# Optimization experiments

Measured on AMD Instinct MI355X. Metric: run time of the kernel, lower is better.

The kernel has to match this reference:

```python
import jax, jax.numpy as jnp
import numpy as np

B, N, IN, OUT, H = 8, 1024, 256, 256, 4
D = OUT // H  # head_dim = 64


def setup_inputs() -> dict:
    key = jax.random.key(0)
    k1, k2, k3, k4 = jax.random.split(key, 4)
    h = jax.random.normal(k1, (B, N, IN), dtype=jnp.float32)
    # torch Linear weight: [out, in], Wh = h @ W.T
    W = jax.random.normal(k2, (H * D, IN), dtype=jnp.float32) * (1.0 / np.sqrt(IN))
    # attention vector a: [n_heads, 2*head_dim] (xavier-uniform-ish scale)
    a = jax.random.normal(k3, (H, 2 * D), dtype=jnp.float32) * 0.1
    adj_mask = jax.random.bernoulli(k4, 0.1, (B, N, N))
    # ensure every row has at least one neighbor (self-loop) to avoid all -inf rows
    adj_mask = adj_mask | jnp.eye(N, dtype=bool)[None]
    return {"h": h, "W": W, "a": a, "adj_mask": adj_mask}


def reference(h, W, a, adj_mask):
    # Wh: [B, H, N, D]
    Wh = (h @ W.T).reshape(B, N, H, D).transpose(0, 2, 1, 3)
    # Split 'a' into src/dst halves: e_ij = leaky_relu(a_src.Wh_i + a_dst.Wh_j)
    # (mathematically identical to the original concat+einsum, without the N^2*2D tensor)
    src = jnp.einsum('bhnd,hd->bhn', Wh, a[:, :D])
    dst = jnp.einsum('bhnd,hd->bhn', Wh, a[:, D:])
    e = jax.nn.leaky_relu(src[:, :, :, None] + dst[:, :, None, :], negative_slope=0.2)
    e = jnp.where(adj_mask[:, None, :, :], e, -jnp.inf)
    att = jax.nn.softmax(e, axis=-1)
    att = jnp.where(jnp.isnan(att), 0.0, att)
    # dropout in eval mode -> identity
    h_prime = jnp.einsum('bhij,bhjd->bhid', att, Wh)
    # concat=True: [B, N, H*D]
    return h_prime.transpose(0, 2, 1, 3).reshape(B, N, H * D)
```

## Files before the change

kernel.cpp:

```cpp
#include <hip/hip_runtime.h>
#include <hip/hip_bf16.h>

#define B 8
#define N 1024
#define IN 256
#define H 4
#define D 64
#define O 256
#define BN (B*N)

typedef __attribute__((ext_vector_type(4))) float f32x4;
typedef __attribute__((ext_vector_type(8))) short short8;
typedef __attribute__((ext_vector_type(4))) short short4v;

__device__ __forceinline__ short f2bf(float f){
  __hip_bfloat16 b = __float2bfloat16(f);
  return __builtin_bit_cast(short, b);
}
__device__ __forceinline__ float bf2f(short s){
  unsigned u = ((unsigned)(unsigned short)s) << 16;
  return __builtin_bit_cast(float, u);
}

__global__ __launch_bounds__(256) void k_wh(const float* __restrict__ hmat,
                                            const float* __restrict__ Wmat,
                                            short* __restrict__ VT){
  const int t = threadIdx.x;
  const int wave = t >> 6, lane = t & 63, quad = lane >> 4, l16 = lane & 15;
  const int msub = blockIdx.x * 32 + (wave >> 1) * 16;
  const int obase = (wave & 1) * 128;
  f32x4 acc[8];
  #pragma unroll
  for(int x=0;x<8;x++) acc[x] = (f32x4){0.f,0.f,0.f,0.f};
  const float* ap = hmat + (size_t)(msub + l16) * IN + quad * 8;
  for(int k0 = 0; k0 < IN; k0 += 32){
    float4 a0 = *(const float4*)(ap + k0);
    float4 a1 = *(const float4*)(ap + k0 + 4);
    short8 A;
    A[0]=f2bf(a0.x); A[1]=f2bf(a0.y); A[2]=f2bf(a0.z); A[3]=f2bf(a0.w);
    A[4]=f2bf(a1.x); A[5]=f2bf(a1.y); A[6]=f2bf(a1.z); A[7]=f2bf(a1.w);
    #pragma unroll
    for(int dt=0; dt<8; dt++){
      const float* bp = Wmat + (size_t)(obase + dt*16 + l16) * IN + k0 + quad*8;
      float4 b0 = *(const float4*)bp;
      float4 b1 = *(const float4*)(bp + 4);
      short8 Bf;
      Bf[0]=f2bf(b0.x); Bf[1]=f2bf(b0.y); Bf[2]=f2bf(b0.z); Bf[3]=f2bf(b0.w);
      Bf[4]=f2bf(b1.x); Bf[5]=f2bf(b1.y); Bf[6]=f2bf(b1.z); Bf[7]=f2bf(b1.w);
      acc[dt] = __builtin_amdgcn_mfma_f32_16x16x32_bf16(A, Bf, acc[dt], 0, 0, 0);
    }
  }
  const int bb = msub >> 10;
  const int nb = (msub & (N-1)) + quad * 4;
  #pragma unroll
  for(int dt=0; dt<8; dt++){
    int o = obase + dt*16 + l16;
    int hh = o >> 6, d = o & 63;
    short4v pk;
    pk[0]=f2bf(acc[dt][0]); pk[1]=f2bf(acc[dt][1]);
    pk[2]=f2bf(acc[dt][2]); pk[3]=f2bf(acc[dt][3]);
    *(short4v*)(VT + (((size_t)(bb*H + hh)*D + d) << 10) + nb) = pk;
  }
}

__global__ __launch_bounds__(256) void k_srcdst(const short* __restrict__ VT,
                                                const float* __restrict__ avec,
                                                float* __restrict__ src,
                                                float* __restrict__ dst){
  int t = blockIdx.x * 256 + threadIdx.x;
  int bh = t >> 10, n = t & (N-1);
  int hh = bh & (H-1);
  const float* av = avec + hh * (2*D);
  const short* vp = VT + ((size_t)bh << 16) + n;
  float s = 0.f, dd = 0.f;
  #pragma unroll 8
  for(int d=0; d<D; d++){
    float v = bf2f(vp[(size_t)d << 10]);
    s  += v * av[d];
    dd += v * av[D + d];
  }
  src[t] = s; dst[t] = dd;
}

__global__ __launch_bounds__(256) void k_attn(const short* __restrict__ VT,
                                              const float* __restrict__ src,
                                              const float* __restrict__ dst,
                                              const int* __restrict__ adj,
                                              float* __restrict__ out){
  __shared__ float dsh[N];
  __shared__ short vt[D * 40];
  __shared__ float lsh[4][16];
  const int t = threadIdx.x;
  const int wave = t >> 6, lane = t & 63, quad = lane >> 4, l16 = lane & 15;
  const int b = blockIdx.z, hh = blockIdx.y;
  const int bh = b * H + hh;
  const int i0 = blockIdx.x * 64;
  for(int j = t; j < N; j += 256) dsh[j] = dst[(size_t)bh * N + j];
  const int i = i0 + wave * 16 + l16;
  const float si = src[(size_t)bh * N + i];
  const int* adjrow = adj + ((size_t)b * N + i) * N;
  const int sd = t >> 2;
  const int sc = (t & 3) * 8;
  const short* vsrc = VT + (((size_t)bh * D + sd) << 10) + sc;
  f32x4 acc[4];
  #pragma unroll
  for(int x=0;x<4;x++) acc[x] = (f32x4){0.f,0.f,0.f,0.f};
  float lsum = 0.f;
  for(int j0 = 0; j0 < N; j0 += 32){
    __syncthreads();
    *(short8*)&vt[sd * 40 + sc] = *(const short8*)(vsrc + j0);
    __syncthreads();
    const int4* amp = (const int4*)(adjrow + j0 + quad * 8);
    int4 m0 = amp[0], m1 = amp[1];
    int msk[8] = {m0.x, m0.y, m0.z, m0.w, m1.x, m1.y, m1.z, m1.w};
    short8 P;
    #pragma unroll
    for(int jj=0; jj<8; jj++){
      float e = si + dsh[j0 + quad*8 + jj];
      e = e > 0.f ? e : 0.2f * e;
      float p = msk[jj] ? __expf(e) : 0.f;
      P[jj] = f2bf(p);
      lsum += bf2f(P[jj]);
    }
    #pragma unroll
    for(int dt=0; dt<4; dt++){
      short8 Bf = *(const short8*)&vt[(dt*16 + l16) * 40 + quad*8];
      acc[dt] = __builtin_amdgcn_mfma_f32_16x16x32_bf16(P, Bf, acc[dt], 0, 0, 0);
    }
  }
  lsum += __shfl_xor(lsum, 16, 64);
  lsum += __shfl_xor(lsum, 32, 64);
  if(quad == 0) lsh[wave][l16] = lsum;
  __syncthreads();
  #pragma unroll
  for(int dt=0; dt<4; dt++){
    #pragma unroll
    for(int r=0; r<4; r++){
      int irow = quad * 4 + r;
      float inv = 1.0f / lsh[wave][irow];
      int ig = i0 + wave * 16 + irow;
      out[((size_t)b * N + ig) * O + hh * D + dt * 16 + l16] = acc[dt][r] * inv;
    }
  }
}

extern "C" void kernel_launch(void* const* d_in, const int* in_sizes, int n_in,
                              void* d_out, int out_size, void* d_ws, size_t ws_size,
                              hipStream_t stream) {
  const float* hmat = (const float*)d_in[0];
  const float* Wmat = (const float*)d_in[1];
  const float* avec = (const float*)d_in[2];
  const int* adj    = (const int*)d_in[3];
  float* out = (float*)d_out;
  short* VT  = (short*)d_ws;
  float* src = (float*)((char*)d_ws + (size_t)4*1024*1024);
  float* dst = src + (size_t)B*H*N;
  k_wh<<<BN/32, 256, 0, stream>>>(hmat, Wmat, VT);
  k_srcdst<<<(B*H*N)/256, 256, 0, stream>>>(VT, avec, src, dst);
  k_attn<<<dim3(N/64, H, B), 256, 0, stream>>>(VT, src, dst, adj, out);
}
```

Baseline: 154.0 us.

## Pack adjacency to bitmask, pre-convert to bf16, fuse src/dst, split-K attention

Adds a prep kernel that packs the int32 adjacency mask into bits and converts h and W to bf16 once. The projection GEMM now computes the src/dst attention dot products in its epilogue, which removes a separate kernel. The attention kernel is split into two j-halves, reads V directly from global memory instead of staging it in shared memory, and writes partial sums that a new combine kernel reduces. The intent is to stop re-reading the 4-byte mask once per head and to increase the number of blocks, at the cost of an extra pass and the partial-sum traffic.

Result: faster. 138.1 us (-10.3%).

```diff
diff --git a/kernel.cpp b/kernel.cpp
--- a/kernel.cpp
+++ b/kernel.cpp
@@ -22,126 +22,179 @@
   return __builtin_bit_cast(float, u);
 }
 
-__global__ __launch_bounds__(256) void k_wh(const float* __restrict__ hmat,
-                                            const float* __restrict__ Wmat,
-                                            short* __restrict__ VT){
+#define PACK_BLOCKS 1024
+#define CVT_BLOCKS  1056
+#define H_ELEMS (BN*IN)
+__global__ __launch_bounds__(256) void k_prep(const int* __restrict__ adj,
+                                              unsigned* __restrict__ bits,
+                                              const float* __restrict__ hmat,
+                                              const float* __restrict__ Wmat,
+                                              short* __restrict__ hbf,
+                                              short* __restrict__ wbf){
+  if(blockIdx.x < PACK_BLOCKS){
+    int t = blockIdx.x * 256 + threadIdx.x;
+    const int4* p = (const int4*)(adj + ((size_t)t << 5));
+    unsigned word = 0;
+    #pragma unroll
+    for(int k = 0; k < 8; k++){
+      int4 m = p[k];
+      word |= (m.x != 0 ? 1u : 0u) << (k*4 + 0);
+      word |= (m.y != 0 ? 1u : 0u) << (k*4 + 1);
+      word |= (m.z != 0 ? 1u : 0u) << (k*4 + 2);
+      word |= (m.w != 0 ? 1u : 0u) << (k*4 + 3);
+    }
+    bits[t] = word;
+  } else {
+    int idx = (blockIdx.x - PACK_BLOCKS) * 256 + threadIdx.x;
+    int e = idx * 8;
+    const float* srcp; short* dstp;
+    if(e < H_ELEMS){ srcp = hmat + e; dstp = hbf + e; }
+    else           { srcp = Wmat + (e - H_ELEMS); dstp = wbf + (e - H_ELEMS); }
+    float4 a0 = *(const float4*)srcp;
+    float4 a1 = *(const float4*)(srcp + 4);
+    short8 pk;
+    pk[0]=f2bf(a0.x); pk[1]=f2bf(a0.y); pk[2]=f2bf(a0.z); pk[3]=f2bf(a0.w);
+    pk[4]=f2bf(a1.x); pk[5]=f2bf(a1.y); pk[6]=f2bf(a1.z); pk[7]=f2bf(a1.w);
+    *(short8*)dstp = pk;
+  }
+}
+
+__global__ __launch_bounds__(256) void k_wh(const short* __restrict__ hbf,
+                                            const short* __restrict__ wbf,
+                                            const float* __restrict__ avec,
+                                            short* __restrict__ VT,
+                                            float* __restrict__ src,
+                                            float* __restrict__ dst){
   const int t = threadIdx.x;
-  const int wave = t >> 6, lane = t & 63, quad = lane >> 4, l16 = lane & 15;
-  const int msub = blockIdx.x * 32 + (wave >> 1) * 16;
-  const int obase = (wave & 1) * 128;
-  f32x4 acc[8];
-  #pragma unroll
-  for(int x=0;x<8;x++) acc[x] = (f32x4){0.f,0.f,0.f,0.f};
-  const float* ap = hmat + (size_t)(msub + l16) * IN + quad * 8;
-  for(int k0 = 0; k0 < IN; k0 += 32){
-    float4 a0 = *(const float4*)(ap + k0);
-    float4 a1 = *(const float4*)(ap + k0 + 4);
-    short8 A;
-    A[0]=f2bf(a0.x); A[1]=f2bf(a0.y); A[2]=f2bf(a0.z); A[3]=f2bf(a0.w);
-    A[4]=f2bf(a1.x); A[5]=f2bf(a1.y); A[6]=f2bf(a1.z); A[7]=f2bf(a1.w);
-    #pragma unroll
-    for(int dt=0; dt<8; dt++){
-      const float* bp = Wmat + (size_t)(obase + dt*16 + l16) * IN + k0 + quad*8;
-      float4 b0 = *(const float4*)bp;
-      float4 b1 = *(const float4*)(bp + 4);
-      short8 Bf;
-      Bf[0]=f2bf(b0.x); Bf[1]=f2bf(b0.y); Bf[2]=f2bf(b0.z); Bf[3]=f2bf(b0.w);
-      Bf[4]=f2bf(b1.x); Bf[5]=f2bf(b1.y); Bf[6]=f2bf(b1.z); Bf[7]=f2bf(b1.w);
+  const int hh = t >> 6, lane = t & 63, quad = lane >> 4, l16 = lane & 15;
+  const int mbase = blockIdx.x * 16;
+  f32x4 acc[4];
+  #pragma unroll
+  for(int x=0;x<4;x++) acc[x] = (f32x4){0.f,0.f,0.f,0.f};
+  const short* ap = hbf + (size_t)(mbase + l16) * IN + quad * 8;
+  const short* bp0 = wbf + (size_t)(hh * 64 + l16) * IN + quad * 8;
+  #pragma unroll
+  for(int kk = 0; kk < 8; kk++){
+    const int k0 = kk * 32;
+    short8 A = *(const short8*)(ap + k0);
+    #pragma unroll
+    for(int dt=0; dt<4; dt++){
+      short8 Bf = *(const short8*)(bp0 + (size_t)dt*16*IN + k0);
       acc[dt] = __builtin_amdgcn_mfma_f32_16x16x32_bf16(A, Bf, acc[dt], 0, 0, 0);
     }
   }
-  const int bb = msub >> 10;
-  const int nb = (msub & (N-1)) + quad * 4;
-  #pragma unroll
-  for(int dt=0; dt<8; dt++){
-    int o = obase + dt*16 + l16;
-    int hh = o >> 6, d = o & 63;
+  const int bb = mbase >> 10;
+  const int nb = (mbase & (N-1)) + quad * 4;
+  const int bh = bb * H + hh;
+  #pragma unroll
+  for(int dt=0; dt<4; dt++){
+    int d = dt*16 + l16;
     short4v pk;
     pk[0]=f2bf(acc[dt][0]); pk[1]=f2bf(acc[dt][1]);
     pk[2]=f2bf(acc[dt][2]); pk[3]=f2bf(acc[dt][3]);
-    *(short4v*)(VT + (((size_t)(bb*H + hh)*D + d) << 10) + nb) = pk;
-  }
-}
-
-__global__ __launch_bounds__(256) void k_srcdst(const short* __restrict__ VT,
-                                                const float* __restrict__ avec,
-                                                float* __restrict__ src,
-                                                float* __restrict__ dst){
-  int t = blockIdx.x * 256 + threadIdx.x;
-  int bh = t >> 10, n = t & (N-1);
-  int hh = bh & (H-1);
-  const float* av = avec + hh * (2*D);
-  const short* vp = VT + ((size_t)bh << 16) + n;
-  float s = 0.f, dd = 0.f;
-  #pragma unroll 8
-  for(int d=0; d<D; d++){
-    float v = bf2f(vp[(size_t)d << 10]);
-    s  += v * av[d];
-    dd += v * av[D + d];
-  }
-  src[t] = s; dst[t] = dd;
+    *(short4v*)(VT + (((size_t)bh * D + d) << 10) + nb) = pk;
+  }
+  float as[4], ad[4];
+  #pragma unroll
+  for(int dt=0; dt<4; dt++){
+    as[dt] = avec[hh*(2*D) + dt*16 + l16];
+    ad[dt] = avec[hh*(2*D) + D + dt*16 + l16];
+  }
+  #pragma unroll
+  for(int r=0; r<4; r++){
+    float s = 0.f, dd = 0.f;
+    #pragma unroll
+    for(int dt=0; dt<4; dt++){ s += acc[dt][r]*as[dt]; dd += acc[dt][r]*ad[dt]; }
+    #pragma unroll
+    for(int off=1; off<16; off<<=1){
+      s  += __shfl_xor(s, off, 64);
+      dd += __shfl_xor(dd, off, 64);
+    }
+    if(l16 == 0){
+      int n = nb + r;
+      src[(size_t)bh * N + n] = s;
+      dst[(size_t)bh * N + n] = dd;
+    }
+  }
 }
 
 __global__ __launch_bounds__(256) void k_attn(const short* __restrict__ VT,
                                               const float* __restrict__ src,
                                               const float* __restrict__ dst,
-                                              const int* __restrict__ adj,
-                                              float* __restrict__ out){
-  __shared__ float dsh[N];
-  __shared__ short vt[D * 40];
-  __shared__ float lsh[4][16];
+                                              const unsigned* __restrict__ bits,
+                                              float* __restrict__ pacc,
+                                              float* __restrict__ plsum){
+  __shared__ float dsh[512];
   const int t = threadIdx.x;
   const int wave = t >> 6, lane = t & 63, quad = lane >> 4, l16 = lane & 15;
   const int b = blockIdx.z, hh = blockIdx.y;
   const int bh = b * H + hh;
-  const int i0 = blockIdx.x * 64;
-  for(int j = t; j < N; j += 256) dsh[j] = dst[(size_t)bh * N + j];
+  const int ib = blockIdx.x >> 1, jc = blockIdx.x & 1;
+  const int i0 = ib * 64, jbase = jc * 512;
+  #pragma unroll
+  for(int j = t; j < 512; j += 256) dsh[j] = dst[(size_t)bh * N + jbase + j];
   const int i = i0 + wave * 16 + l16;
   const float si = src[(size_t)bh * N + i];
-  const int* adjrow = adj + ((size_t)b * N + i) * N;
-  const int sd = t >> 2;
-  const int sc = (t & 3) * 8;
-  const short* vsrc = VT + (((size_t)bh * D + sd) << 10) + sc;
+  const int4* mp = (const int4*)(bits + ((size_t)b * N + i) * 32 + jc * 16);
+  int4 mv0 = mp[0], mv1 = mp[1], mv2 = mp[2], mv3 = mp[3];
+  unsigned mw[16] = {(unsigned)mv0.x,(unsigned)mv0.y,(unsigned)mv0.z,(unsigned)mv0.w,
+                     (unsigned)mv1.x,(unsigned)mv1.y,(unsigned)mv1.z,(unsigned)mv1.w,
+                     (unsigned)mv2.x,(unsigned)mv2.y,(unsigned)mv2.z,(unsigned)mv2.w,
+                     (unsigned)mv3.x,(unsigned)mv3.y,(unsigned)mv3.z,(unsigned)mv3.w};
+  const short* vrow = VT + (((size_t)bh * D) << 10) + jbase + quad * 8;
   f32x4 acc[4];
   #pragma unroll
   for(int x=0;x<4;x++) acc[x] = (f32x4){0.f,0.f,0.f,0.f};
   float lsum = 0.f;
-  for(int j0 = 0; j0 < N; j0 += 32){
-    __syncthreads();
-    *(short8*)&vt[sd * 40 + sc] = *(const short8*)(vsrc + j0);
-    __syncthreads();
-    const int4* amp = (const int4*)(adjrow + j0 + quad * 8);
-    int4 m0 = amp[0], m1 = amp[1];
-    int msk[8] = {m0.x, m0.y, m0.z, m0.w, m1.x, m1.y, m1.z, m1.w};
+  __syncthreads();
+  #pragma unroll
+  for(int jt = 0; jt < 16; jt++){
+    const int j0 = jt * 32;
+    const unsigned word = mw[jt];
+    float4 d0 = *(const float4*)&dsh[j0 + quad*8];
+    float4 d1 = *(const float4*)&dsh[j0 + quad*8 + 4];
+    float dv[8] = {d0.x,d0.y,d0.z,d0.w,d1.x,d1.y,d1.z,d1.w};
     short8 P;
     #pragma unroll
     for(int jj=0; jj<8; jj++){
-      float e = si + dsh[j0 + quad*8 + jj];
-      e = e > 0.f ? e : 0.2f * e;
-      float p = msk[jj] ? __expf(e) : 0.f;
+      float e = si + dv[jj];
+      e = fmaxf(e, 0.2f * e);
+      float p = ((word >> (quad*8 + jj)) & 1u) ? __expf(e) : 0.f;
       P[jj] = f2bf(p);
       lsum += bf2f(P[jj]);
     }
     #pragma unroll
     for(int dt=0; dt<4; dt++){
-      short8 Bf = *(const short8*)&vt[(dt*16 + l16) * 40 + quad*8];
+      short8 Bf = *(const short8*)(vrow + (((size_t)(dt*16 + l16)) << 10) + j0);
       acc[dt] = __builtin_amdgcn_mfma_f32_16x16x32_bf16(P, Bf, acc[dt], 0, 0, 0);
     }
   }
   lsum += __shfl_xor(lsum, 16, 64);
   lsum += __shfl_xor(lsum, 32, 64);
-  if(quad == 0) lsh[wave][l16] = lsum;
-  __syncthreads();
+  const int pslot = bh * 2 + jc;
+  if(quad == 0) plsum[(size_t)pslot * N + i] = lsum;
+  float* pa = pacc + ((size_t)pslot << 16);
   #pragma unroll
   for(int dt=0; dt<4; dt++){
     #pragma unroll
     for(int r=0; r<4; r++){
-      int irow = quad * 4 + r;
-      float inv = 1.0f / lsh[wave][irow];
-      int ig = i0 + wave * 16 + irow;
-      out[((size_t)b * N + ig) * O + hh * D + dt * 16 + l16] = acc[dt][r] * inv;
-    }
-  }
+      int ig = i0 + wave*16 + quad*4 + r;
+      pa[(ig << 6) + dt*16 + l16] = acc[dt][r];
+    }
+  }
+}
+
+__global__ __launch_bounds__(256) void k_combine(const float* __restrict__ pacc,
+                                                 const float* __restrict__ plsum,
+                                                 float* __restrict__ out){
+  int t = blockIdx.x * 256 + threadIdx.x;
+  int o = t & 255, n = (t >> 8) & (N-1), b = t >> 18;
+  int hh = o >> 6, d = o & 63;
+  int slot = (b * H + hh) * 2;
+  size_t base = ((size_t)slot << 16) + (n << 6) + d;
+  float p = pacc[base] + pacc[base + 65536];
+  float l = plsum[(size_t)slot * N + n] + plsum[(size_t)(slot+1) * N + n];
+  out[t] = p / l;
 }
 
 extern "C" void kernel_launch(void* const* d_in, const int* in_sizes, int n_in,
@@ -152,10 +205,17 @@
   const float* avec = (const float*)d_in[2];
   const int* adj    = (const int*)d_in[3];
   float* out = (float*)d_out;
-  short* VT  = (short*)d_ws;
-  float* src = (float*)((char*)d_ws + (size_t)4*1024*1024);
-  float* dst = src + (size_t)B*H*N;
-  k_wh<<<BN/32, 256, 0, stream>>>(hmat, Wmat, VT);
-  k_srcdst<<<(B*H*N)/256, 256, 0, stream>>>(VT, avec, src, dst);
-  k_attn<<<dim3(N/64, H, B), 256, 0, stream>>>(VT, src, dst, adj, out);
-}
+  char* ws = (char*)d_ws;
+  short*    VT    = (short*)   (ws);
+  short*    hbf   = (short*)   (ws + (size_t) 4*1024*1024);
+  short*    wbf   = (short*)   (ws + (size_t) 8*1024*1024);
+  unsigned* bits  = (unsigned*)(ws + (size_t) 9*1024*1024);
+  float*    src   = (float*)   (ws + (size_t)10*1024*1024);
+  float*    dst   = (float*)   (ws + (size_t)10*1024*1024 + 131072);
+  float*    plsum = (float*)   (ws + (size_t)11*1024*1024);
+  float*    pacc  = (float*)   (ws + (size_t)12*1024*1024);
+  k_prep<<<PACK_BLOCKS + CVT_BLOCKS, 256, 0, stream>>>(adj, bits, hmat, Wmat, hbf, wbf);
+  k_wh<<<BN/16, 256, 0, stream>>>(hbf, wbf, avec, VT, src, dst);
+  k_attn<<<dim3(32, H, B), 256, 0, stream>>>(VT, src, dst, bits, pacc, plsum);
+  k_combine<<<(BN*O)/256, 256, 0, stream>>>(pacc, plsum, out);
+}
```
